# Performance work log

Measured on AMD Instinct MI355X. Metric: run time of the kernel, lower is better.

The kernel has to match this reference:

```python
import jax, jax.numpy as jnp
import numpy as np

B, S, D = 8, 2048, 512

def setup_inputs() -> dict:
    key = jax.random.key(0)
    ks = jax.random.split(key, 9)
    scale = 1.0 / np.sqrt(D)
    return {
        "x": jax.random.normal(ks[0], (B, S, D), dtype=jnp.float32),
        "attention_mask": jax.random.uniform(ks[1], (B, S), dtype=jnp.float32),
        "Wq": jax.random.normal(ks[2], (D, D), dtype=jnp.float32) * scale,
        "bq": jax.random.normal(ks[3], (D,), dtype=jnp.float32) * 0.01,
        "Wk": jax.random.normal(ks[4], (D, D), dtype=jnp.float32) * scale,
        "bk": jax.random.normal(ks[5], (D,), dtype=jnp.float32) * 0.01,
        "Wv": jax.random.normal(ks[6], (D, D), dtype=jnp.float32) * scale,
        "bv": jax.random.normal(ks[7], (D,), dtype=jnp.float32) * 0.01,
    }

def reference(x, attention_mask, Wq, bq, Wk, bk, Wv, bv):
    # Single-head self-attention, full O(S^2) scores as in the original.
    q = jnp.einsum('bsd,df->bsf', x, Wq) + bq  # [B,S,D]
    k = jnp.einsum('bsd,df->bsf', x, Wk) + bk
    v = jnp.einsum('bsd,df->bsf', x, Wv) + bv
    scores = jnp.einsum('bqd,bkd->bqk', q, k) / jnp.sqrt(jnp.float32(D))  # [B,S,S]
    attn = jax.nn.softmax(scores, axis=2)
    weighted = jnp.einsum('bqk,bkd->bqd', attn, v)  # [B,S,D]
    # mask applied multiplicatively to the output, per original code
    return weighted * attention_mask[:, :, None]
```

## Files before the change

kernel.cpp:

```cpp
#include <hip/hip_runtime.h>
#include <math.h>
#include <stdint.h>


typedef _Float16 f16x8 __attribute__((ext_vector_type(8)));
typedef _Float16 f16x4 __attribute__((ext_vector_type(4)));
typedef _Float16 f16x2 __attribute__((ext_vector_type(2)));
typedef float f32x4 __attribute__((ext_vector_type(4)));
typedef float f32x16 __attribute__((ext_vector_type(16)));

__device__ __forceinline__ void async16(const _Float16* g, _Float16* l) {
    __builtin_amdgcn_global_load_lds(
        (const __attribute__((address_space(1))) unsigned int*)(uintptr_t)g,
        (__attribute__((address_space(3))) unsigned int*)(unsigned int)(uintptr_t)l,
        16, 0, 0);
}

__device__ __forceinline__ float frag_sum8(f16x8 v, float acc) {
#if __has_builtin(__builtin_amdgcn_fdot2)
    const f16x2 one2 = {(_Float16)1.f, (_Float16)1.f};
    const f16x2* p = (const f16x2*)&v;
    acc = __builtin_amdgcn_fdot2(p[0], one2, acc, false);
    acc = __builtin_amdgcn_fdot2(p[1], one2, acc, false);
    acc = __builtin_amdgcn_fdot2(p[2], one2, acc, false);
    acc = __builtin_amdgcn_fdot2(p[3], one2, acc, false);
#else
#pragma unroll
    for (int j = 0; j < 8; j++) acc += (float)v[j];
#endif
    return acc;
}

#define MFMA32(a, b, c) __builtin_amdgcn_mfma_f32_32x32x16_f16(a, b, c, 0, 0, 0)
#define BAR() __builtin_amdgcn_s_barrier()
#define LGKM0() asm volatile("s_waitcnt lgkmcnt(0)" ::: "memory")

template <int NT, bool WITH_RS>
__device__ __forceinline__ void core128sq(
    const _Float16* __restrict__ A, const _Float16* __restrict__ B,
    int ld, int row0, int col0, _Float16* sm, f32x16 acc[2][2], float rs[2])
{
    const int tid = threadIdx.x, lane = tid & 63, wave = tid >> 6;
    const int wm = wave >> 1, wn = wave & 1;
    const int rc = lane >> 3;
    const int l7 = lane & 7;
    const int fr32 = lane & 31, q2 = lane >> 5;
    const int fx = fr32 & 7;
    const int rq = (lane >> 3) & 3;

    const _Float16* gA[4]; int lA[4];
#pragma unroll
    for (int i = 0; i < 4; i++) {
        int c = wave * 4 + i;
        int swz = ((l7 ^ rc ^ (c & 3)) * 8);
        gA[i] = A + (size_t)(row0 + 8 * c + rc) * ld + swz;
        lA[i] = c * 512;
    }
    const _Float16* gBe[2]; const _Float16* gBl[2]; int lBe[2], lBl[2];
#pragma unroll
    for (int i = 0; i < 2; i++) {
        int idx = wave * 2 + i;
        int je = (idx & 3) + (idx >> 2) * 8;
        int jl = je + 4;
        int swze = ((l7 ^ rc ^ (je & 3)) * 8);
        int swzl = ((l7 ^ rc ^ (jl & 3)) * 8);
        gBe[i] = B + (size_t)(col0 + 8 * je + rc) * ld + swze;
        gBl[i] = B + (size_t)(col0 + 8 * jl + rc) * ld + swzl;
        lBe[i] = 8192 + je * 512;
        lBl[i] = 8192 + jl * 512;
    }

#pragma unroll
    for (int i = 0; i < 4; i++) async16(gA[i], sm + lA[i]);
#pragma unroll
    for (int i = 0; i < 2; i++) async16(gBe[i], sm + lBe[i]);
#pragma unroll
    for (int i = 0; i < 2; i++) async16(gBl[i], sm + lBl[i]);
#pragma unroll
    for (int i = 0; i < 4; i++) async16(gA[i] + 64, sm + 16384 + lA[i]);
#pragma unroll
    for (int i = 0; i < 2; i++) async16(gBe[i] + 64, sm + 16384 + lBe[i]);
    asm volatile("s_waitcnt vmcnt(6)" ::: "memory");
    BAR();

#pragma unroll 2
    for (int t = 0; t < NT; ++t) {
        const _Float16* As = sm + (t & 1) * 16384;
        const _Float16* Bs = As + 8192;
        f16x8 af[2][4], bf[4];

#pragma unroll
        for (int m = 0; m < 2; m++)
#pragma unroll
            for (int s = 0; s < 4; s++) {
                int ra = wm * 64 + m * 32 + fr32;
                af[m][s] = *(const f16x8*)&As[ra * 64 + ((((2 * s + q2) ^ fx ^ rq)) * 8)];
            }
#pragma unroll
        for (int s = 0; s < 4; s++) {
            int rb = wn * 64 + fr32;
            bf[s] = *(const f16x8*)&Bs[rb * 64 + ((((2 * s + q2) ^ fx ^ rq)) * 8)];
        }
        if (t + 1 < NT) {
            _Float16* nb = sm + ((t + 1) & 1) * 16384;
#pragma unroll
            for (int i = 0; i < 2; i++)
                async16(gBl[i] + (t + 1) * 64, nb + lBl[i]);
        }
        BAR(); LGKM0();
        if (WITH_RS) {
#pragma unroll
            for (int m = 0; m < 2; m++)
#pragma unroll
                for (int s = 0; s < 4; s++) rs[m] = frag_sum8(af[m][s], rs[m]);
        }
        __builtin_amdgcn_s_setprio(1);
#pragma unroll
        for (int s = 0; s < 4; s++)
#pragma unroll
            for (int m = 0; m < 2; m++)
                acc[m][0] = MFMA32(af[m][s], bf[s], acc[m][0]);
        __builtin_amdgcn_s_setprio(0);
        BAR();

#pragma unroll
        for (int s = 0; s < 4; s++) {
            int rb = wn * 64 + 32 + fr32;
            bf[s] = *(const f16x8*)&Bs[rb * 64 + ((((2 * s + q2) ^ fx ^ rq)) * 8)];
        }
        if (t + 2 < NT) {
            _Float16* stg = sm + (t & 1) * 16384;
            const int k2 = (t + 2) * 64;
#pragma unroll
            for (int i = 0; i < 4; i++) async16(gA[i] + k2, stg + lA[i]);
#pragma unroll
            for (int i = 0; i < 2; i++) async16(gBe[i] + k2, stg + lBe[i]);
            asm volatile("s_waitcnt vmcnt(6)" ::: "memory");
        } else {
            asm volatile("s_waitcnt vmcnt(0)" ::: "memory");
        }
        BAR(); LGKM0();
        __builtin_amdgcn_s_setprio(1);
#pragma unroll
        for (int s = 0; s < 4; s++)
#pragma unroll
            for (int m = 0; m < 2; m++)
                acc[m][1] = MFMA32(af[m][s], bf[s], acc[m][1]);
        __builtin_amdgcn_s_setprio(0);
        BAR();
    }
}

__global__ __launch_bounds__(256) void prep(
    const float* __restrict__ x,
    const float* __restrict__ Wq, const float* __restrict__ Wk,
    const float* __restrict__ Wv,
    _Float16* __restrict__ Xh,
    _Float16* __restrict__ WqT, _Float16* __restrict__ WkT,
    _Float16* __restrict__ WvT)
{
    const int bid = blockIdx.x;
    if (bid < 8192) {
        int i = (bid * 256 + threadIdx.x) * 4;
        float4 v = *(const float4*)(x + i);
        f16x4 h;
        h.x = (_Float16)v.x; h.y = (_Float16)v.y;
        h.z = (_Float16)v.z; h.w = (_Float16)v.w;
        *(f16x4*)&Xh[i] = h;
    } else {
        int t = bid - 8192;
        int z = t >> 10;
        const float* W = (z == 0) ? Wq : (z == 1) ? Wk : Wv;
        _Float16* Wt   = (z == 0) ? WqT : (z == 1) ? WkT : WvT;
        int idx = (t & 1023) * 256 + threadIdx.x;
        int n = idx >> 9, k = idx & 511;
        Wt[idx] = (_Float16)W[k * 512 + n];
    }
}

__global__ __launch_bounds__(256, 2) void proj_mfma(
    const _Float16* __restrict__ Xh,
    const _Float16* __restrict__ WqT, const float* __restrict__ bq,
    const _Float16* __restrict__ WkT, const float* __restrict__ bk,
    const _Float16* __restrict__ WvT, const float* __restrict__ bv,
    _Float16* __restrict__ Qh, _Float16* __restrict__ Kh,
    _Float16* __restrict__ Vt)
{
    __shared__ __align__(16) _Float16 smem[2 * 16384];
    const int z = blockIdx.z;
    f32x16 acc[2][2] = {};
    float rs_unused[2];

    const int lane = threadIdx.x & 63, wave = threadIdx.x >> 6;
    const int wm = wave >> 1, wn = wave & 1;
    const int fr32 = lane & 31, q2 = lane >> 5;

    if (z < 2) {
        const _Float16* Wt = (z == 0) ? WqT : WkT;
        const float* bias  = (z == 0) ? bq : bk;
        _Float16* P        = (z == 0) ? Qh : Kh;
        const float sc     = (z == 0) ? 0.04419417382415922f : 1.0f;
        const int row0 = blockIdx.x * 128, col0 = blockIdx.y * 128;
        core128sq<8, false>(Xh, Wt, 512, row0, col0, smem, acc, rs_unused);
#pragma unroll
        for (int mf = 0; mf < 2; mf++)
#pragma unroll
            for (int nf = 0; nf < 2; nf++) {
                int col = col0 + wn * 64 + nf * 32 + fr32;
                float bb = bias[col];
#pragma unroll
                for (int reg = 0; reg < 16; reg++) {
                    int row = row0 + wm * 64 + mf * 32 +
                              (reg & 3) + 8 * (reg >> 2) + 4 * q2;
                    P[(size_t)row * 512 + col] = (_Float16)((acc[mf][nf][reg] + bb) * sc);
                }
            }
    } else {
        const int row0 = blockIdx.y * 128;
        const int col0 = blockIdx.x * 128;
        core128sq<8, false>(WvT, Xh, 512, row0, col0, smem, acc, rs_unused);
#pragma unroll
        for (int mf = 0; mf < 2; mf++)
#pragma unroll
            for (int nf = 0; nf < 2; nf++) {
                int col = col0 + wn * 64 + nf * 32 + fr32;
                size_t obase = (size_t)(col >> 11) * (512 * 2048) + (col & 2047);
#pragma unroll
                for (int reg = 0; reg < 16; reg++) {
                    int row = row0 + wm * 64 + mf * 32 +
                              (reg & 3) + 8 * (reg >> 2) + 4 * q2;
                    Vt[obase + (size_t)row * 2048] = (_Float16)(acc[mf][nf][reg] + bv[row]);
                }
            }
    }
}

__global__ __launch_bounds__(256, 2) void scores_mfma(
    const _Float16* __restrict__ Qh, const _Float16* __restrict__ Kh,
    _Float16* __restrict__ Sh)
{
    __shared__ __align__(16) _Float16 smem[2 * 16384];
    const int bid = blockIdx.x;
    const int b   = bid & 7;
    const int rem = bid >> 3;
    const int col0 = (rem & 15) * 128;
    const int row0 = (rem >> 4) * 128;

    const _Float16* A = Qh + (size_t)b * 2048 * 512;
    const _Float16* B = Kh + (size_t)b * 2048 * 512;
    _Float16* S = Sh + (size_t)b * 2048 * 2048;

    f32x16 acc[2][2] = {};
    float rs_unused[2];

    core128sq<8, false>(A, B, 512, row0, col0, smem, acc, rs_unused);

    const int lane = threadIdx.x & 63, wave = threadIdx.x >> 6;
    const int wm = wave >> 1, wn = wave & 1;
    const int fr32 = lane & 31, q2 = lane >> 5;
#pragma unroll
    for (int mf = 0; mf < 2; mf++)
#pragma unroll
        for (int nf = 0; nf < 2; nf++) {
            int col = col0 + wn * 64 + nf * 32 + fr32;
#pragma unroll
            for (int reg = 0; reg < 16; reg++) {
                int row = row0 + wm * 64 + mf * 32 +
                          (reg & 3) + 8 * (reg >> 2) + 4 * q2;
                S[(size_t)row * 2048 + col] = (_Float16)__expf(acc[mf][nf][reg]);
            }
        }
}

__global__ __launch_bounds__(256, 2) void av_mfma(
    const _Float16* __restrict__ Sh, const _Float16* __restrict__ Vt,
    const float* __restrict__ mask, float* __restrict__ out)
{
    __shared__ __align__(16) _Float16 smem[2 * 16384];
    const int bid = blockIdx.x;
    const int b   = bid & 7;
    const int rem = bid >> 3;
    const int col0 = (rem & 3) * 128;
    const int row0 = (rem >> 2) * 128;

    const _Float16* A = Sh + (size_t)b * 2048 * 2048;
    const _Float16* B = Vt + (size_t)b * 512 * 2048;
    float* O = out + (size_t)b * 2048 * 512;
    const float* mk = mask + (size_t)b * 2048;

    f32x16 acc[2][2] = {};
    float rs[2] = {0.f, 0.f};

    core128sq<32, true>(A, B, 2048, row0, col0, smem, acc, rs);

    const int lane = threadIdx.x & 63, wave = threadIdx.x >> 6;
    const int wm = wave >> 1, wn = wave & 1;
    const int fr32 = lane & 31, q2 = lane >> 5;

#pragma unroll
    for (int mf = 0; mf < 2; mf++) rs[mf] += __shfl_xor(rs[mf], 32, 64);
    __syncthreads();
    float* l_s = (float*)smem;
    if (wn == 0 && lane < 32) {
#pragma unroll
        for (int mf = 0; mf < 2; mf++) l_s[wm * 64 + mf * 32 + lane] = rs[mf];
    }
    __syncthreads();

#pragma unroll
    for (int mf = 0; mf < 2; mf++)
#pragma unroll
        for (int nf = 0; nf < 2; nf++) {
            int col = col0 + wn * 64 + nf * 32 + fr32;
#pragma unroll
            for (int reg = 0; reg < 16; reg++) {
                int lrow = wm * 64 + mf * 32 + (reg & 3) + 8 * (reg >> 2) + 4 * q2;
                int row = row0 + lrow;
                float s = mk[row] / l_s[lrow];
                O[(size_t)row * 512 + col] = acc[mf][nf][reg] * s;
            }
        }
}

extern "C" void kernel_launch(void* const* d_in, const int* in_sizes, int n_in,
                              void* d_out, int out_size, void* d_ws, size_t ws_size,
                              hipStream_t stream) {
    const float* x    = (const float*)d_in[0];
    const float* mask = (const float*)d_in[1];
    const float* Wq   = (const float*)d_in[2];
    const float* bq   = (const float*)d_in[3];
    const float* Wk   = (const float*)d_in[4];
    const float* bk   = (const float*)d_in[5];
    const float* Wv   = (const float*)d_in[6];
    const float* bv   = (const float*)d_in[7];
    float* out = (float*)d_out;

    const size_t BSD = (size_t)8 * 2048 * 512;
    _Float16* base = (_Float16*)d_ws;
    _Float16* Qh  = base;
    _Float16* Kh  = Qh + BSD;
    _Float16* Vt  = Kh + BSD;
    _Float16* WqT = Vt + BSD;
    _Float16* WkT = WqT + 512 * 512;
    _Float16* WvT = WkT + 512 * 512;
    _Float16* Xh  = WvT + 512 * 512;
    _Float16* Sh  = Xh;

    prep<<<dim3(8192 + 3 * 1024), dim3(256), 0, stream>>>(
        x, Wq, Wk, Wv, Xh, WqT, WkT, WvT);
    proj_mfma<<<dim3(128, 4, 3), dim3(256), 0, stream>>>(
        Xh, WqT, bq, WkT, bk, WvT, bv, Qh, Kh, Vt);
    scores_mfma<<<dim3(2048), dim3(256), 0, stream>>>(Qh, Kh, Sh);
    av_mfma<<<dim3(512), dim3(256), 0, stream>>>(Sh, Vt, mask, out);
}
```

Measured before the change: 214.6 us.

## Move softmax row sums into scores epilogue via atomics; use 16x16 MFMA in AV

The softmax denominator is now accumulated in the scores kernel epilogue, using wave shuffles plus global atomicAdd into a zeroed lsum buffer. This removes the per-fragment fdot2 row-sum work from the AV inner loop. The AV GEMM also switches from 32x32x16 to 16x16x32 MFMA tiles with a new core routine and matching epilogue. In exchange the scores kernel gains extra reductions and atomic traffic, and the 16x16 layout needs more accumulator registers.

```diff
diff --git a/kernel.cpp b/kernel.cpp
--- a/kernel.cpp
+++ b/kernel.cpp
@@ -5,7 +5,6 @@
 
 typedef _Float16 f16x8 __attribute__((ext_vector_type(8)));
 typedef _Float16 f16x4 __attribute__((ext_vector_type(4)));
-typedef _Float16 f16x2 __attribute__((ext_vector_type(2)));
 typedef float f32x4 __attribute__((ext_vector_type(4)));
 typedef float f32x16 __attribute__((ext_vector_type(16)));
 
@@ -16,29 +15,129 @@
         16, 0, 0);
 }
 
-__device__ __forceinline__ float frag_sum8(f16x8 v, float acc) {
-#if __has_builtin(__builtin_amdgcn_fdot2)
-    const f16x2 one2 = {(_Float16)1.f, (_Float16)1.f};
-    const f16x2* p = (const f16x2*)&v;
-    acc = __builtin_amdgcn_fdot2(p[0], one2, acc, false);
-    acc = __builtin_amdgcn_fdot2(p[1], one2, acc, false);
-    acc = __builtin_amdgcn_fdot2(p[2], one2, acc, false);
-    acc = __builtin_amdgcn_fdot2(p[3], one2, acc, false);
-#else
-#pragma unroll
-    for (int j = 0; j < 8; j++) acc += (float)v[j];
-#endif
-    return acc;
-}
-
+#define MFMA16(a, b, c) __builtin_amdgcn_mfma_f32_16x16x32_f16(a, b, c, 0, 0, 0)
 #define MFMA32(a, b, c) __builtin_amdgcn_mfma_f32_32x32x16_f16(a, b, c, 0, 0, 0)
 #define BAR() __builtin_amdgcn_s_barrier()
 #define LGKM0() asm volatile("s_waitcnt lgkmcnt(0)" ::: "memory")
 
-template <int NT, bool WITH_RS>
-__device__ __forceinline__ void core128sq(
+template <int NT>
+__device__ __forceinline__ void core16(
     const _Float16* __restrict__ A, const _Float16* __restrict__ B,
-    int ld, int row0, int col0, _Float16* sm, f32x16 acc[2][2], float rs[2])
+    int ld, int row0, int col0, _Float16* sm, f32x4 acc[4][4])
+{
+    const int tid = threadIdx.x, lane = tid & 63, wave = tid >> 6;
+    const int wm = wave >> 1, wn = wave & 1;
+    const int rc = lane >> 3;
+    const int swz = ((lane & 7) ^ rc) * 8;
+    const int fr = lane & 15, q = lane >> 4, fx = fr & 7;
+    const size_t laneoff = (size_t)rc * ld + swz;
+
+    const _Float16* gA[4]; int lA[4];
+#pragma unroll
+    for (int i = 0; i < 4; i++) {
+        int c = wave * 4 + i;
+        gA[i] = A + (size_t)(row0 + 8 * c) * ld + laneoff;
+        lA[i] = c * 512;
+    }
+    const _Float16* gBe[2]; const _Float16* gBl[2]; int lBe[2], lBl[2];
+#pragma unroll
+    for (int i = 0; i < 2; i++) {
+        int idx = wave * 2 + i;
+        int je = (idx & 3) + (idx >> 2) * 8;
+        int jl = je + 4;
+        gBe[i] = B + (size_t)(col0 + 8 * je) * ld + laneoff;
+        gBl[i] = B + (size_t)(col0 + 8 * jl) * ld + laneoff;
+        lBe[i] = 8192 + je * 512;
+        lBl[i] = 8192 + jl * 512;
+    }
+
+#pragma unroll
+    for (int i = 0; i < 4; i++) async16(gA[i], sm + lA[i]);
+#pragma unroll
+    for (int i = 0; i < 2; i++) async16(gBe[i], sm + lBe[i]);
+#pragma unroll
+    for (int i = 0; i < 2; i++) async16(gBl[i], sm + lBl[i]);
+#pragma unroll
+    for (int i = 0; i < 4; i++) async16(gA[i] + 64, sm + 16384 + lA[i]);
+#pragma unroll
+    for (int i = 0; i < 2; i++) async16(gBe[i] + 64, sm + 16384 + lBe[i]);
+    asm volatile("s_waitcnt vmcnt(6)" ::: "memory");
+    BAR();
+
+#pragma unroll 2
+    for (int t = 0; t < NT; ++t) {
+        const _Float16* As = sm + (t & 1) * 16384;
+        const _Float16* Bs = As + 8192;
+        f16x8 af[4][2], b0f[2][2], b1f[2][2];
+
+#pragma unroll
+        for (int m = 0; m < 4; m++)
+#pragma unroll
+            for (int s = 0; s < 2; s++) {
+                int ra = wm * 64 + m * 16 + fr;
+                af[m][s] = *(const f16x8*)&As[ra * 64 + (((s * 4 + q) ^ fx) * 8)];
+            }
+#pragma unroll
+        for (int n = 0; n < 2; n++)
+#pragma unroll
+            for (int s = 0; s < 2; s++) {
+                int rb = wn * 64 + n * 16 + fr;
+                b0f[n][s] = *(const f16x8*)&Bs[rb * 64 + (((s * 4 + q) ^ fx) * 8)];
+            }
+        if (t + 1 < NT) {
+            _Float16* nb = sm + ((t + 1) & 1) * 16384;
+#pragma unroll
+            for (int i = 0; i < 2; i++)
+                async16(gBl[i] + (t + 1) * 64, nb + lBl[i]);
+        }
+        BAR(); LGKM0();
+        __builtin_amdgcn_s_setprio(1);
+#pragma unroll
+        for (int s = 0; s < 2; s++)
+#pragma unroll
+            for (int m = 0; m < 4; m++)
+#pragma unroll
+                for (int n = 0; n < 2; n++)
+                    acc[m][n] = MFMA16(af[m][s], b0f[n][s], acc[m][n]);
+        __builtin_amdgcn_s_setprio(0);
+        BAR();
+
+#pragma unroll
+        for (int n = 0; n < 2; n++)
+#pragma unroll
+            for (int s = 0; s < 2; s++) {
+                int rb = wn * 64 + (2 + n) * 16 + fr;
+                b1f[n][s] = *(const f16x8*)&Bs[rb * 64 + (((s * 4 + q) ^ fx) * 8)];
+            }
+        if (t + 2 < NT) {
+            _Float16* stg = sm + (t & 1) * 16384;
+            const int k2 = (t + 2) * 64;
+#pragma unroll
+            for (int i = 0; i < 4; i++) async16(gA[i] + k2, stg + lA[i]);
+#pragma unroll
+            for (int i = 0; i < 2; i++) async16(gBe[i] + k2, stg + lBe[i]);
+            asm volatile("s_waitcnt vmcnt(6)" ::: "memory");
+        } else {
+            asm volatile("s_waitcnt vmcnt(0)" ::: "memory");
+        }
+        BAR(); LGKM0();
+        __builtin_amdgcn_s_setprio(1);
+#pragma unroll
+        for (int s = 0; s < 2; s++)
+#pragma unroll
+            for (int m = 0; m < 4; m++)
+#pragma unroll
+                for (int n = 0; n < 2; n++)
+                    acc[m][2 + n] = MFMA16(af[m][s], b1f[n][s], acc[m][2 + n]);
+        __builtin_amdgcn_s_setprio(0);
+        BAR();
+    }
+}
+
+template <int NT>
+__device__ __forceinline__ void core32(
+    const _Float16* __restrict__ A, const _Float16* __restrict__ B,
+    int ld, int row0, int col0, _Float16* sm, f32x16 acc[2][2])
 {
     const int tid = threadIdx.x, lane = tid & 63, wave = tid >> 6;
     const int wm = wave >> 1, wn = wave & 1;
@@ -108,12 +207,6 @@
                 async16(gBl[i] + (t + 1) * 64, nb + lBl[i]);
         }
         BAR(); LGKM0();
-        if (WITH_RS) {
-#pragma unroll
-            for (int m = 0; m < 2; m++)
-#pragma unroll
-                for (int s = 0; s < 4; s++) rs[m] = frag_sum8(af[m][s], rs[m]);
-        }
         __builtin_amdgcn_s_setprio(1);
 #pragma unroll
         for (int s = 0; s < 4; s++)
@@ -157,7 +250,7 @@
     const float* __restrict__ Wv,
     _Float16* __restrict__ Xh,
     _Float16* __restrict__ WqT, _Float16* __restrict__ WkT,
-    _Float16* __restrict__ WvT)
+    _Float16* __restrict__ WvT, float* __restrict__ lsum)
 {
     const int bid = blockIdx.x;
     if (bid < 8192) {
@@ -167,7 +260,7 @@
         h.x = (_Float16)v.x; h.y = (_Float16)v.y;
         h.z = (_Float16)v.z; h.w = (_Float16)v.w;
         *(f16x4*)&Xh[i] = h;
-    } else {
+    } else if (bid < 11264) {
         int t = bid - 8192;
         int z = t >> 10;
         const float* W = (z == 0) ? Wq : (z == 1) ? Wk : Wv;
@@ -175,6 +268,9 @@
         int idx = (t & 1023) * 256 + threadIdx.x;
         int n = idx >> 9, k = idx & 511;
         Wt[idx] = (_Float16)W[k * 512 + n];
+    } else {
+        int i = ((bid - 11264) * 256 + threadIdx.x) * 4;
+        *(float4*)(lsum + i) = (float4){0.f, 0.f, 0.f, 0.f};
     }
 }
 
@@ -189,7 +285,6 @@
     __shared__ __align__(16) _Float16 smem[2 * 16384];
     const int z = blockIdx.z;
     f32x16 acc[2][2] = {};
-    float rs_unused[2];
 
     const int lane = threadIdx.x & 63, wave = threadIdx.x >> 6;
     const int wm = wave >> 1, wn = wave & 1;
@@ -201,7 +296,7 @@
         _Float16* P        = (z == 0) ? Qh : Kh;
         const float sc     = (z == 0) ? 0.04419417382415922f : 1.0f;
         const int row0 = blockIdx.x * 128, col0 = blockIdx.y * 128;
-        core128sq<8, false>(Xh, Wt, 512, row0, col0, smem, acc, rs_unused);
+        core32<8>(Xh, Wt, 512, row0, col0, smem, acc);
 #pragma unroll
         for (int mf = 0; mf < 2; mf++)
 #pragma unroll
@@ -218,7 +313,7 @@
     } else {
         const int row0 = blockIdx.y * 128;
         const int col0 = blockIdx.x * 128;
-        core128sq<8, false>(WvT, Xh, 512, row0, col0, smem, acc, rs_unused);
+        core32<8>(WvT, Xh, 512, row0, col0, smem, acc);
 #pragma unroll
         for (int mf = 0; mf < 2; mf++)
 #pragma unroll
@@ -237,7 +332,7 @@
 
 __global__ __launch_bounds__(256, 2) void scores_mfma(
     const _Float16* __restrict__ Qh, const _Float16* __restrict__ Kh,
-    _Float16* __restrict__ Sh)
+    _Float16* __restrict__ Sh, float* __restrict__ lsum)
 {
     __shared__ __align__(16) _Float16 smem[2 * 16384];
     const int bid = blockIdx.x;
@@ -249,15 +344,22 @@
     const _Float16* A = Qh + (size_t)b * 2048 * 512;
     const _Float16* B = Kh + (size_t)b * 2048 * 512;
     _Float16* S = Sh + (size_t)b * 2048 * 2048;
+    float* lb = lsum + (size_t)b * 2048;
 
     f32x16 acc[2][2] = {};
-    float rs_unused[2];
-
-    core128sq<8, false>(A, B, 512, row0, col0, smem, acc, rs_unused);
+
+    core32<8>(A, B, 512, row0, col0, smem, acc);
 
     const int lane = threadIdx.x & 63, wave = threadIdx.x >> 6;
     const int wm = wave >> 1, wn = wave & 1;
     const int fr32 = lane & 31, q2 = lane >> 5;
+
+    float rsum[2][16];
+#pragma unroll
+    for (int mf = 0; mf < 2; mf++)
+#pragma unroll
+        for (int reg = 0; reg < 16; reg++) rsum[mf][reg] = 0.f;
+
 #pragma unroll
     for (int mf = 0; mf < 2; mf++)
 #pragma unroll
@@ -267,14 +369,39 @@
             for (int reg = 0; reg < 16; reg++) {
                 int row = row0 + wm * 64 + mf * 32 +
                           (reg & 3) + 8 * (reg >> 2) + 4 * q2;
-                S[(size_t)row * 2048 + col] = (_Float16)__expf(acc[mf][nf][reg]);
-            }
-        }
+                _Float16 h = (_Float16)__expf(acc[mf][nf][reg]);
+                S[(size_t)row * 2048 + col] = h;
+                rsum[mf][reg] += (float)h;
+            }
+        }
+#pragma unroll
+    for (int mf = 0; mf < 2; mf++)
+#pragma unroll
+        for (int reg = 0; reg < 16; reg++) {
+            float v = rsum[mf][reg];
+            v += __shfl_xor(v, 1, 64);
+            v += __shfl_xor(v, 2, 64);
+            v += __shfl_xor(v, 4, 64);
+            v += __shfl_xor(v, 8, 64);
+            v += __shfl_xor(v, 16, 64);
+            rsum[mf][reg] = v;
+        }
+    if (fr32 == 0) {
+#pragma unroll
+        for (int mf = 0; mf < 2; mf++)
+#pragma unroll
+            for (int reg = 0; reg < 16; reg++) {
+                int row = row0 + wm * 64 + mf * 32 +
+                          (reg & 3) + 8 * (reg >> 2) + 4 * q2;
+                atomicAdd(&lb[row], rsum[mf][reg]);
+            }
+    }
 }
 
 __global__ __launch_bounds__(256, 2) void av_mfma(
     const _Float16* __restrict__ Sh, const _Float16* __restrict__ Vt,
-    const float* __restrict__ mask, float* __restrict__ out)
+    const float* __restrict__ mask, const float* __restrict__ lsum,
+    float* __restrict__ out)
 {
     __shared__ __align__(16) _Float16 smem[2 * 16384];
     const int bid = blockIdx.x;
@@ -287,37 +414,30 @@
     const _Float16* B = Vt + (size_t)b * 512 * 2048;
     float* O = out + (size_t)b * 2048 * 512;
     const float* mk = mask + (size_t)b * 2048;
-
-    f32x16 acc[2][2] = {};
-    float rs[2] = {0.f, 0.f};
-
-    core128sq<32, true>(A, B, 2048, row0, col0, smem, acc, rs);
+    const float* lb = lsum + (size_t)b * 2048;
+
+    f32x4 acc[4][4];
+#pragma unroll
+    for (int i = 0; i < 4; i++)
+#pragma unroll
+        for (int j = 0; j < 4; j++) acc[i][j] = (f32x4){0.f, 0.f, 0.f, 0.f};
+
+    core16<32>(A, B, 2048, row0, col0, smem, acc);
 
     const int lane = threadIdx.x & 63, wave = threadIdx.x >> 6;
     const int wm = wave >> 1, wn = wave & 1;
-    const int fr32 = lane & 31, q2 = lane >> 5;
-
-#pragma unroll
-    for (int mf = 0; mf < 2; mf++) rs[mf] += __shfl_xor(rs[mf], 32, 64);
-    __syncthreads();
-    float* l_s = (float*)smem;
-    if (wn == 0 && lane < 32) {
-#pragma unroll
-        for (int mf = 0; mf < 2; mf++) l_s[wm * 64 + mf * 32 + lane] = rs[mf];
-    }
-    __syncthreads();
-
-#pragma unroll
-    for (int mf = 0; mf < 2; mf++)
-#pragma unroll
-        for (int nf = 0; nf < 2; nf++) {
-            int col = col0 + wn * 64 + nf * 32 + fr32;
-#pragma unroll
-            for (int reg = 0; reg < 16; reg++) {
-                int lrow = wm * 64 + mf * 32 + (reg & 3) + 8 * (reg >> 2) + 4 * q2;
-                int row = row0 + lrow;
-                float s = mk[row] / l_s[lrow];
-                O[(size_t)row * 512 + col] = acc[mf][nf][reg] * s;
+    const int er = (lane >> 4) * 4, ec = lane & 15;
+
+#pragma unroll
+    for (int tm = 0; tm < 4; tm++)
+#pragma unroll
+        for (int r = 0; r < 4; r++) {
+            int row = row0 + wm * 64 + tm * 16 + er + r;
+            float s = mk[row] / lb[row];
+#pragma unroll
+            for (int tn = 0; tn < 4; tn++) {
+                int col = col0 + wn * 64 + tn * 16 + ec;
+                O[(size_t)row * 512 + col] = acc[tm][tn][r] * s;
             }
         }
 }
@@ -336,6 +456,7 @@
     float* out = (float*)d_out;
 
     const size_t BSD = (size_t)8 * 2048 * 512;
+    const size_t SSZ = (size_t)8 * 2048 * 2048;
     _Float16* base = (_Float16*)d_ws;
     _Float16* Qh  = base;
     _Float16* Kh  = Qh + BSD;
@@ -345,11 +466,12 @@
     _Float16* WvT = WkT + 512 * 512;
     _Float16* Xh  = WvT + 512 * 512;
     _Float16* Sh  = Xh;
-
-    prep<<<dim3(8192 + 3 * 1024), dim3(256), 0, stream>>>(
-        x, Wq, Wk, Wv, Xh, WqT, WkT, WvT);
+    float*    lsum = (float*)(Sh + SSZ);
+
+    prep<<<dim3(8192 + 3 * 1024 + 16), dim3(256), 0, stream>>>(
+        x, Wq, Wk, Wv, Xh, WqT, WkT, WvT, lsum);
     proj_mfma<<<dim3(128, 4, 3), dim3(256), 0, stream>>>(
         Xh, WqT, bq, WkT, bk, WvT, bv, Qh, Kh, Vt);
-    scores_mfma<<<dim3(2048), dim3(256), 0, stream>>>(Qh, Kh, Sh);
-    av_mfma<<<dim3(512), dim3(256), 0, stream>>>(Sh, Vt, mask, out);
-}
+    scores_mfma<<<dim3(2048), dim3(256), 0, stream>>>(Qh, Kh, Sh, lsum);
+    av_mfma<<<dim3(512), dim3(256), 0, stream>>>(Sh, Vt, mask, lsum, out);
+}
```

Result: slower. 276.1 us (+28.7%).
